# Kernel optimization log

Hardware: AMD Instinct MI355X
Metric: run time of the kernel (lower is better)

The kernel has to match this reference:

```python
import jax, jax.numpy as jnp
import numpy as np

DIM = 512
NUM_HEADS = 8
HEAD_DIM = DIM // NUM_HEADS
REL_POS_BINS = 961
B, N = 64, 256


def setup_inputs() -> dict:
    key = jax.random.key(0)
    ks = jax.random.split(key, 7)
    x = jax.random.normal(ks[0], (B, N, DIM), dtype=jnp.float32)
    rel_pos_index = jax.random.randint(ks[1], (N, N), 0, REL_POS_BINS)
    s = 1.0 / np.sqrt(DIM)
    qkv_w = jax.random.normal(ks[2], (3 * DIM, DIM), dtype=jnp.float32) * s
    qkv_b = jax.random.normal(ks[3], (3 * DIM,), dtype=jnp.float32) * 0.02
    proj_w = jax.random.normal(ks[4], (DIM, DIM), dtype=jnp.float32) * s
    proj_b = jax.random.normal(ks[5], (DIM,), dtype=jnp.float32) * 0.02
    rel_pos_bias = jax.random.normal(ks[6], (NUM_HEADS, REL_POS_BINS), dtype=jnp.float32) * 0.02
    return {"x": x, "rel_pos_index": rel_pos_index, "qkv_w": qkv_w,
            "qkv_b": qkv_b, "proj_w": proj_w, "proj_b": proj_b,
            "rel_pos_bias": rel_pos_bias}


def reference(x, rel_pos_index, qkv_w, qkv_b, proj_w, proj_b, rel_pos_bias):
    Bn, Nn, C = x.shape
    H, D = NUM_HEADS, HEAD_DIM
    qkv = x @ qkv_w.T + qkv_b                      # (B,N,3C)
    qkv = qkv.reshape(Bn, Nn, 3, H, D).transpose(2, 0, 3, 1, 4)  # (3,B,H,N,D)
    q, k, v = qkv[0], qkv[1], qkv[2]
    scale = 1.0 / jnp.sqrt(jnp.asarray(D, dtype=x.dtype))
    scores = jnp.einsum('bhnd,bhmd->bhnm', q, k) * scale          # (B,H,N,N)
    bias = rel_pos_bias[:, rel_pos_index]                          # (H,N,N) gather
    scores = scores + bias[None]
    attn = jax.nn.softmax(scores, axis=-1)
    out = jnp.einsum('bhnm,bhmd->bhnd', attn, v)                   # (B,H,N,D)
    out = out.transpose(0, 2, 1, 3).reshape(Bn, Nn, C)
    return out @ proj_w.T + proj_b
```

## Files before the change

### kernel.cpp

```cpp
#include <hip/hip_runtime.h>
#include <stdint.h>

#define DIM 512
#define NHEADS 8
#define HDIM 64
#define NBINS 961
#define BATCH 64
#define SEQ 256
#define NTOK (BATCH*SEQ)
#define BHND (BATCH*NHEADS*SEQ*HDIM)

using bf16x8 = __attribute__((ext_vector_type(8))) short;
using f32x4  = __attribute__((ext_vector_type(4))) float;

__device__ __forceinline__ unsigned short f2bf(float f) {
  unsigned u = __float_as_uint(f);
  u += 0x7FFF + ((u >> 16) & 1);
  return (unsigned short)(u >> 16);
}

__device__ __forceinline__ void async16(const void* g, void* lds) {
  __builtin_amdgcn_global_load_lds(
      (const __attribute__((address_space(1))) unsigned int*)g,
      (__attribute__((address_space(3))) unsigned int*)lds,
      16, 0, 0);
}


__global__ void cast_kernel(const float* __restrict__ in,
                            unsigned short* __restrict__ out, int n4) {
  int i = blockIdx.x * 256 + threadIdx.x;
  if (i >= n4) return;
  float4 f = reinterpret_cast<const float4*>(in)[i];
  ushort4 o;
  o.x = f2bf(f.x); o.y = f2bf(f.y); o.z = f2bf(f.z); o.w = f2bf(f.w);
  reinterpret_cast<ushort4*>(out)[i] = o;
}

__global__ void bias_kernel(const int* __restrict__ idx,
                            const float* __restrict__ rpb,
                            float* __restrict__ bf) {
  int i = blockIdx.x * 256 + threadIdx.x;
  if (i >= NHEADS * SEQ * SEQ) return;
  int h = i >> 16;
  int r = i & 65535;
  bf[i] = rpb[h * NBINS + idx[r]];
}


__device__ __forceinline__ void stage_tile(const unsigned short* __restrict__ A,
                                           const unsigned short* __restrict__ Bw,
                                           char* gsm, int buf, int T,
                                           int m0, int n0, int t, int wv) {
  char* As = gsm + buf * 16384;
  char* Bs = As + 8192;
  const int kk = T * 32;
#pragma unroll
  for (int i = 0; i < 2; ++i) {
    int c = t + i * 256;
    int row = c >> 2, ch = c & 3;
    int sch = ch ^ ((row >> 1) & 3);
    const unsigned short* ga = A + (size_t)(m0 + row) * 512 + kk + sch * 8;
    async16(ga, As + (i * 256 + wv * 64) * 16);
    const unsigned short* gb = Bw + (size_t)(n0 + row) * 512 + kk + sch * 8;
    async16(gb, Bs + (i * 256 + wv * 64) * 16);
  }
}

template<int EPI>
__global__ __launch_bounds__(256) void gemm_bt(
    const unsigned short* __restrict__ A,
    const unsigned short* __restrict__ Bw,
    const float* __restrict__ bias,
    void* __restrict__ outp) {
  __shared__ char gsm[32768];
  const int t = threadIdx.x;
  const int lane = t & 63;
  const int l15 = lane & 15, lg = lane >> 4;
  const int m0 = blockIdx.x * 128, n0 = blockIdx.y * 128;
  const int wv = t >> 6;
  const int wm = wv & 1, wn = wv >> 1;

  f32x4 acc[4][4];
  const f32x4 fz = {0.f, 0.f, 0.f, 0.f};
#pragma unroll
  for (int a = 0; a < 4; ++a)
#pragma unroll
    for (int b = 0; b < 4; ++b) acc[a][b] = fz;

  stage_tile(A, Bw, gsm, 0, 0, m0, n0, t, wv);
  stage_tile(A, Bw, gsm, 1, 1, m0, n0, t, wv);

#pragma unroll 2
  for (int T = 0; T < 16; ++T) {
    if (T < 15) asm volatile("s_waitcnt vmcnt(4)" ::: "memory");
    else        asm volatile("s_waitcnt vmcnt(0)" ::: "memory");
    __builtin_amdgcn_s_barrier();
    __builtin_amdgcn_sched_barrier(0);

    char* As = gsm + (T & 1) * 16384;
    char* Bs = As + 8192;
    bf16x8 af[4], bfr[4];
#pragma unroll
    for (int x = 0; x < 4; ++x) {
      int ra = wm * 64 + x * 16 + l15;
      af[x]  = *(const bf16x8*)(As + ra * 64 + ((lg ^ ((ra >> 1) & 3)) * 16));
      int rb = wn * 64 + x * 16 + l15;
      bfr[x] = *(const bf16x8*)(Bs + rb * 64 + ((lg ^ ((rb >> 1) & 3)) * 16));
    }
    asm volatile("s_waitcnt lgkmcnt(0)" ::: "memory");
    __builtin_amdgcn_sched_barrier(0);
    __builtin_amdgcn_s_barrier();

    if (T < 14) stage_tile(A, Bw, gsm, T & 1, T + 2, m0, n0, t, wv);
    __builtin_amdgcn_sched_barrier(0);

    __builtin_amdgcn_s_setprio(1);
#pragma unroll
    for (int mi = 0; mi < 4; ++mi)
#pragma unroll
      for (int ni = 0; ni < 4; ++ni)
        acc[mi][ni] = __builtin_amdgcn_mfma_f32_16x16x32_bf16(af[mi], bfr[ni], acc[mi][ni], 0, 0, 0);
    __builtin_amdgcn_s_setprio(0);
  }

#pragma unroll
  for (int mi = 0; mi < 4; ++mi)
#pragma unroll
    for (int ni = 0; ni < 4; ++ni)
#pragma unroll
      for (int r = 0; r < 4; ++r) {
        int row = m0 + wm * 64 + mi * 16 + lg * 4 + r;
        int col = n0 + wn * 64 + ni * 16 + l15;
        float v = acc[mi][ni][r] + bias[col];
        if (EPI == 0) {
          int which = col >> 9, hd = col & 511;
          int b = row >> 8, n = row & 255;
          ((unsigned short*)outp)[(size_t)which * BHND +
              (((size_t)(b * NHEADS + (hd >> 6)) * SEQ + n) * HDIM) + (hd & 63)] = f2bf(v);
        } else {
          ((float*)outp)[(size_t)row * 512 + col] = v;
        }
      }
}


__global__ __launch_bounds__(512, 2) void attn_kernel(
    const unsigned short* __restrict__ qb,
    const unsigned short* __restrict__ kb,
    const unsigned short* __restrict__ vb,
    const float* __restrict__ biasf,
    unsigned short* __restrict__ aout) {
  extern __shared__ char smem[];
  char* k_s = smem;
  char* v_s = smem + 32768;
  const int t = threadIdx.x, lane = t & 63, w = t >> 6;
  const int l15 = lane & 15, lg = lane >> 4;
  char* P_s = smem + 65536 + w * 4096;
  const int bh = blockIdx.x;
  const int h = bh & 7;
  const int b = bh >> 3;
  const size_t base = (size_t)bh * (SEQ * HDIM);

#pragma unroll
  for (int i = 0; i < 4; ++i) {
    int c = i * 512 + t;
    int row = c >> 3, sl = c & 7;
    bf16x8 val = *(const bf16x8*)(kb + base + (size_t)c * 8);
    *(bf16x8*)(k_s + row * 128 + ((sl * 16) ^ ((row & 7) << 4))) = val;
  }
#pragma unroll
  for (int i = 0; i < 4; ++i) {
    int c = i * 512 + t;
    int key = c >> 3, d0 = (c & 7) * 8;
    bf16x8 val = *(const bf16x8*)(vb + base + (size_t)c * 8);
#pragma unroll
    for (int j = 0; j < 8; ++j) {
      int d = d0 + j;
      int term = (((d & 7) ^ ((d >> 3) & 7)) << 4);
      *(short*)(v_s + d * 512 + ((key * 2) ^ term)) = val[j];
    }
  }
  bf16x8 qa[2][2];
#pragma unroll
  for (int rf = 0; rf < 2; ++rf)
#pragma unroll
    for (int ks = 0; ks < 2; ++ks)
      qa[rf][ks] = *(const bf16x8*)(qb + base + (size_t)(w * 32 + rf * 16 + l15) * 64 + ks * 32 + lg * 8);
  __syncthreads();

  f32x4 accs[2][16];
  const f32x4 fz = {0.f, 0.f, 0.f, 0.f};
#pragma unroll
  for (int a = 0; a < 2; ++a)
#pragma unroll
    for (int c = 0; c < 16; ++c) accs[a][c] = fz;
  __builtin_amdgcn_s_setprio(1);
#pragma unroll
  for (int cf = 0; cf < 16; ++cf) {
    int key = cf * 16 + l15;
#pragma unroll
    for (int ks = 0; ks < 2; ++ks) {
      bf16x8 kf = *(const bf16x8*)(k_s + key * 128 + ((lg * 16 + ks * 64) ^ ((key & 7) << 4)));
      accs[0][cf] = __builtin_amdgcn_mfma_f32_16x16x32_bf16(qa[0][ks], kf, accs[0][cf], 0, 0, 0);
      accs[1][cf] = __builtin_amdgcn_mfma_f32_16x16x32_bf16(qa[1][ks], kf, accs[1][cf], 0, 0, 0);
    }
  }
  __builtin_amdgcn_s_setprio(0);

  const float* bh_ptr = biasf + h * 65536;
#pragma unroll
  for (int rf = 0; rf < 2; ++rf)
#pragma unroll
    for (int r = 0; r < 4; ++r) {
      int n = w * 32 + rf * 16 + lg * 4 + r;
      const float* bp = bh_ptr + n * 256 + l15;
#pragma unroll
      for (int cf = 0; cf < 16; ++cf)
        accs[rf][cf][r] = accs[rf][cf][r] * 0.125f + bp[cf * 16];
    }

  float pinv[2][4];
#pragma unroll
  for (int rf = 0; rf < 2; ++rf)
#pragma unroll
    for (int r = 0; r < 4; ++r) {
      float m = -1e30f;
#pragma unroll
      for (int cf = 0; cf < 16; ++cf) m = fmaxf(m, accs[rf][cf][r]);
#pragma unroll
      for (int off = 1; off < 16; off <<= 1) m = fmaxf(m, __shfl_xor(m, off, 64));
      float s = 0.f;
#pragma unroll
      for (int cf = 0; cf < 16; ++cf) {
        float p = __expf(accs[rf][cf][r] - m);
        accs[rf][cf][r] = p;
        s += p;
      }
#pragma unroll
      for (int off = 1; off < 16; off <<= 1) s += __shfl_xor(s, off, 64);
      pinv[rf][r] = 1.0f / s;
    }

  f32x4 acco[2][4];
#pragma unroll
  for (int a = 0; a < 2; ++a)
#pragma unroll
    for (int c2 = 0; c2 < 4; ++c2) acco[a][c2] = fz;

  for (int ch = 0; ch < 4; ++ch) {
#pragma unroll
    for (int rf = 0; rf < 2; ++rf)
#pragma unroll
      for (int cl = 0; cl < 4; ++cl)
#pragma unroll
        for (int r = 0; r < 4; ++r) {
          int rowl = rf * 16 + lg * 4 + r;
          int ml = cl * 16 + l15;
          float p = accs[rf][ch * 4 + cl][r] * pinv[rf][r];
          *(short*)(P_s + rowl * 128 + ((ml * 2) ^ ((rowl & 7) << 4))) = (short)f2bf(p);
        }
#pragma unroll
    for (int ks = 0; ks < 2; ++ks) {
      bf16x8 pa[2];
#pragma unroll
      for (int rf = 0; rf < 2; ++rf) {
        int row = rf * 16 + l15;
        pa[rf] = *(const bf16x8*)(P_s + row * 128 + ((lg * 16 + ks * 64) ^ ((row & 7) << 4)));
      }
      int keyb = (ch * 64 + ks * 32 + lg * 8) * 2;
      __builtin_amdgcn_s_setprio(1);
#pragma unroll
      for (int df = 0; df < 4; ++df) {
        int d = df * 16 + l15;
        int term = (((d & 7) ^ ((d >> 3) & 7)) << 4);
        bf16x8 vf = *(const bf16x8*)(v_s + d * 512 + (keyb ^ term));
        acco[0][df] = __builtin_amdgcn_mfma_f32_16x16x32_bf16(pa[0], vf, acco[0][df], 0, 0, 0);
        acco[1][df] = __builtin_amdgcn_mfma_f32_16x16x32_bf16(pa[1], vf, acco[1][df], 0, 0, 0);
      }
      __builtin_amdgcn_s_setprio(0);
    }
  }

#pragma unroll
  for (int rf = 0; rf < 2; ++rf)
#pragma unroll
    for (int df = 0; df < 4; ++df)
#pragma unroll
      for (int r = 0; r < 4; ++r) {
        int n = w * 32 + rf * 16 + lg * 4 + r;
        int d = df * 16 + l15;
        aout[((size_t)(b * SEQ + n)) * DIM + h * HDIM + d] = f2bf(acco[rf][df][r]);
      }
}


extern "C" void kernel_launch(void* const* d_in, const int* in_sizes, int n_in,
                              void* d_out, int out_size, void* d_ws, size_t ws_size,
                              hipStream_t stream) {
  const float* x      = (const float*)d_in[0];
  const int*   rpi    = (const int*)d_in[1];
  const float* qkv_w  = (const float*)d_in[2];
  const float* qkv_b  = (const float*)d_in[3];
  const float* proj_w = (const float*)d_in[4];
  const float* proj_b = (const float*)d_in[5];
  const float* rpb    = (const float*)d_in[6];

  char* ws = (char*)d_ws;
  unsigned short* xb    = (unsigned short*)ws;
  unsigned short* wqkv  = (unsigned short*)(ws + 16777216);
  unsigned short* wproj = (unsigned short*)(ws + 18350080);
  float*          biasf = (float*)         (ws + 18874368);
  unsigned short* qkvb  = (unsigned short*)(ws + 20971520);
  unsigned short* aoutb = (unsigned short*)(ws + 71303168);

  cast_kernel<<<8192, 256, 0, stream>>>(x, xb, 2097152);
  cast_kernel<<<768, 256, 0, stream>>>(qkv_w, wqkv, 196608);
  cast_kernel<<<256, 256, 0, stream>>>(proj_w, wproj, 65536);
  bias_kernel<<<2048, 256, 0, stream>>>(rpi, rpb, biasf);

  dim3 g1(128, 12);
  gemm_bt<0><<<g1, 256, 0, stream>>>(xb, wqkv, qkv_b, (void*)qkvb);

  attn_kernel<<<512, 512, 98304, stream>>>(qkvb, qkvb + BHND, qkvb + 2 * (size_t)BHND,
                                           biasf, aoutb);

  dim3 g2(128, 4);
  gemm_bt<1><<<g2, 256, 0, stream>>>(aoutb, wproj, proj_b, d_out);
}
```

Baseline: 102.1 us.

## Triple-buffer GEMM staging, read K from global, vectorize bias loads

The GEMM moves from a double-buffered LDS ring to a triple-buffered one, which removes the second barrier per K-step and lets the next tile be issued before the current fragments are read. Occupancy is raised to three blocks per CU. The attention kernel no longer stages K in LDS: each wave reads K fragments straight from global memory, which cuts LDS to 64KB and allows a higher launch-bounds occupancy target. The bias table is rewritten in a permuted layout so each lane can fetch its 16 bias values with four 16-byte vector loads. The costs are redundant global K reads across the 8 waves and extra register pressure from the higher occupancy targets.

```diff
diff --git a/kernel.cpp b/kernel.cpp
--- a/kernel.cpp
+++ b/kernel.cpp
@@ -44,36 +44,36 @@
   if (i >= NHEADS * SEQ * SEQ) return;
   int h = i >> 16;
   int r = i & 65535;
-  bf[i] = rpb[h * NBINS + idx[r]];
+  int n = r >> 8, m = r & 255;
+  bf[(size_t)h * 65536 + n * 256 + (m & 15) * 16 + (m >> 4)] = rpb[h * NBINS + idx[r]];
 }
 
 
 __device__ __forceinline__ void stage_tile(const unsigned short* __restrict__ A,
                                            const unsigned short* __restrict__ Bw,
-                                           char* gsm, int buf, int T,
-                                           int m0, int n0, int t, int wv) {
-  char* As = gsm + buf * 16384;
-  char* Bs = As + 8192;
+                                           char* slot, int T,
+                                           int m0, int n0, int t) {
   const int kk = T * 32;
+  const int wv64 = (t >> 6) << 6;
 #pragma unroll
   for (int i = 0; i < 2; ++i) {
     int c = t + i * 256;
     int row = c >> 2, ch = c & 3;
     int sch = ch ^ ((row >> 1) & 3);
     const unsigned short* ga = A + (size_t)(m0 + row) * 512 + kk + sch * 8;
-    async16(ga, As + (i * 256 + wv * 64) * 16);
+    async16(ga, slot + (i * 256 + wv64) * 16);
     const unsigned short* gb = Bw + (size_t)(n0 + row) * 512 + kk + sch * 8;
-    async16(gb, Bs + (i * 256 + wv * 64) * 16);
+    async16(gb, slot + 8192 + (i * 256 + wv64) * 16);
   }
 }
 
 template<int EPI>
-__global__ __launch_bounds__(256) void gemm_bt(
+__global__ __launch_bounds__(256, 3) void gemm_bt(
     const unsigned short* __restrict__ A,
     const unsigned short* __restrict__ Bw,
     const float* __restrict__ bias,
     void* __restrict__ outp) {
-  __shared__ char gsm[32768];
+  __shared__ char gsm[49152];
   const int t = threadIdx.x;
   const int lane = t & 63;
   const int l15 = lane & 15, lg = lane >> 4;
@@ -88,17 +88,24 @@
 #pragma unroll
     for (int b = 0; b < 4; ++b) acc[a][b] = fz;
 
-  stage_tile(A, Bw, gsm, 0, 0, m0, n0, t, wv);
-  stage_tile(A, Bw, gsm, 1, 1, m0, n0, t, wv);
-
-#pragma unroll 2
+  stage_tile(A, Bw, gsm,         0, m0, n0, t);
+  stage_tile(A, Bw, gsm + 16384, 1, m0, n0, t);
+
+  int cur = 0;
+#pragma unroll 1
   for (int T = 0; T < 16; ++T) {
     if (T < 15) asm volatile("s_waitcnt vmcnt(4)" ::: "memory");
     else        asm volatile("s_waitcnt vmcnt(0)" ::: "memory");
     __builtin_amdgcn_s_barrier();
     __builtin_amdgcn_sched_barrier(0);
 
-    char* As = gsm + (T & 1) * 16384;
+    if (T < 14) {
+      int dst = cur + 2; if (dst >= 3) dst -= 3;
+      stage_tile(A, Bw, gsm + dst * 16384, T + 2, m0, n0, t);
+    }
+    __builtin_amdgcn_sched_barrier(0);
+
+    char* As = gsm + cur * 16384;
     char* Bs = As + 8192;
     bf16x8 af[4], bfr[4];
 #pragma unroll
@@ -110,10 +117,6 @@
     }
     asm volatile("s_waitcnt lgkmcnt(0)" ::: "memory");
     __builtin_amdgcn_sched_barrier(0);
-    __builtin_amdgcn_s_barrier();
-
-    if (T < 14) stage_tile(A, Bw, gsm, T & 1, T + 2, m0, n0, t, wv);
-    __builtin_amdgcn_sched_barrier(0);
 
     __builtin_amdgcn_s_setprio(1);
 #pragma unroll
@@ -122,6 +125,8 @@
       for (int ni = 0; ni < 4; ++ni)
         acc[mi][ni] = __builtin_amdgcn_mfma_f32_16x16x32_bf16(af[mi], bfr[ni], acc[mi][ni], 0, 0, 0);
     __builtin_amdgcn_s_setprio(0);
+
+    cur = cur + 1; if (cur >= 3) cur -= 3;
   }
 
 #pragma unroll
@@ -145,18 +150,17 @@
 }
 
 
-__global__ __launch_bounds__(512, 2) void attn_kernel(
+__global__ __launch_bounds__(512, 4) void attn_kernel(
     const unsigned short* __restrict__ qb,
     const unsigned short* __restrict__ kb,
     const unsigned short* __restrict__ vb,
     const float* __restrict__ biasf,
     unsigned short* __restrict__ aout) {
   extern __shared__ char smem[];
-  char* k_s = smem;
-  char* v_s = smem + 32768;
+  char* v_s = smem;
   const int t = threadIdx.x, lane = t & 63, w = t >> 6;
   const int l15 = lane & 15, lg = lane >> 4;
-  char* P_s = smem + 65536 + w * 4096;
+  char* P_s = smem + 32768 + w * 4096;
   const int bh = blockIdx.x;
   const int h = bh & 7;
   const int b = bh >> 3;
@@ -165,13 +169,6 @@
 #pragma unroll
   for (int i = 0; i < 4; ++i) {
     int c = i * 512 + t;
-    int row = c >> 3, sl = c & 7;
-    bf16x8 val = *(const bf16x8*)(kb + base + (size_t)c * 8);
-    *(bf16x8*)(k_s + row * 128 + ((sl * 16) ^ ((row & 7) << 4))) = val;
-  }
-#pragma unroll
-  for (int i = 0; i < 4; ++i) {
-    int c = i * 512 + t;
     int key = c >> 3, d0 = (c & 7) * 8;
     bf16x8 val = *(const bf16x8*)(vb + base + (size_t)c * 8);
 #pragma unroll
@@ -187,37 +184,38 @@
 #pragma unroll
     for (int ks = 0; ks < 2; ++ks)
       qa[rf][ks] = *(const bf16x8*)(qb + base + (size_t)(w * 32 + rf * 16 + l15) * 64 + ks * 32 + lg * 8);
-  __syncthreads();
-
+
+  const unsigned short* kbase = kb + base;
   f32x4 accs[2][16];
   const f32x4 fz = {0.f, 0.f, 0.f, 0.f};
 #pragma unroll
   for (int a = 0; a < 2; ++a)
 #pragma unroll
     for (int c = 0; c < 16; ++c) accs[a][c] = fz;
-  __builtin_amdgcn_s_setprio(1);
 #pragma unroll
   for (int cf = 0; cf < 16; ++cf) {
     int key = cf * 16 + l15;
 #pragma unroll
     for (int ks = 0; ks < 2; ++ks) {
-      bf16x8 kf = *(const bf16x8*)(k_s + key * 128 + ((lg * 16 + ks * 64) ^ ((key & 7) << 4)));
+      bf16x8 kf = *(const bf16x8*)(kbase + (size_t)key * 64 + ks * 32 + lg * 8);
       accs[0][cf] = __builtin_amdgcn_mfma_f32_16x16x32_bf16(qa[0][ks], kf, accs[0][cf], 0, 0, 0);
       accs[1][cf] = __builtin_amdgcn_mfma_f32_16x16x32_bf16(qa[1][ks], kf, accs[1][cf], 0, 0, 0);
     }
   }
-  __builtin_amdgcn_s_setprio(0);
-
-  const float* bh_ptr = biasf + h * 65536;
+
+  const float* bh_ptr = biasf + (size_t)h * 65536;
 #pragma unroll
   for (int rf = 0; rf < 2; ++rf)
 #pragma unroll
     for (int r = 0; r < 4; ++r) {
       int n = w * 32 + rf * 16 + lg * 4 + r;
-      const float* bp = bh_ptr + n * 256 + l15;
-#pragma unroll
-      for (int cf = 0; cf < 16; ++cf)
-        accs[rf][cf][r] = accs[rf][cf][r] * 0.125f + bp[cf * 16];
+      const f32x4* bp = (const f32x4*)(bh_ptr + n * 256 + l15 * 16);
+      f32x4 b0 = bp[0], b1 = bp[1], b2 = bp[2], b3 = bp[3];
+#pragma unroll
+      for (int cf = 0; cf < 16; ++cf) {
+        float bb = (cf < 4) ? b0[cf] : (cf < 8) ? b1[cf - 4] : (cf < 12) ? b2[cf - 8] : b3[cf - 12];
+        accs[rf][cf][r] = accs[rf][cf][r] * 0.125f + bb;
+      }
     }
 
   float pinv[2][4];
@@ -241,6 +239,8 @@
       for (int off = 1; off < 16; off <<= 1) s += __shfl_xor(s, off, 64);
       pinv[rf][r] = 1.0f / s;
     }
+
+  __syncthreads();
 
   f32x4 acco[2][4];
 #pragma unroll
@@ -322,7 +322,7 @@
   dim3 g1(128, 12);
   gemm_bt<0><<<g1, 256, 0, stream>>>(xb, wqkv, qkv_b, (void*)qkvb);
 
-  attn_kernel<<<512, 512, 98304, stream>>>(qkvb, qkvb + BHND, qkvb + 2 * (size_t)BHND,
+  attn_kernel<<<512, 512, 65536, stream>>>(qkvb, qkvb + BHND, qkvb + 2 * (size_t)BHND,
                                            biasf, aoutb);
 
   dim3 g2(128, 4);
```

Measured after the change: 239.7 us. +134.8%, slower.
